# Performance work log

Measured on AMD Instinct MI355X. Metric: run time of the kernel, lower is better.

The kernel has to match this reference:

```python
import jax, jax.numpy as jnp
import numpy as np

VOCAB = 64
H = 64
B, L = 256, 2048


def setup_inputs() -> dict:
    key = jax.random.key(0)
    ks = jax.random.split(key, 12)
    s = 0.02
    return {
        "seq":   jax.random.randint(ks[0], (B, L), 0, VOCAB),
        "embed": jax.random.normal(ks[1], (VOCAB, H), jnp.float32) * s,
        "W1":    jax.random.normal(ks[2], (H, 2 * H), jnp.float32) * s,
        "b1":    jnp.zeros((2 * H,), jnp.float32),
        "W2":    jax.random.normal(ks[3], (2 * H, H), jnp.float32) * s,
        "b2":    jnp.zeros((H,), jnp.float32),
        "gamma": jnp.ones((H,), jnp.float32),
        "beta":  jnp.zeros((H,), jnp.float32),
        "Wr":    jax.random.normal(ks[4], (H, H), jnp.float32) * s,
        "br":    jnp.zeros((H,), jnp.float32),
        "Wo":    jax.random.normal(ks[5], (H, VOCAB), jnp.float32) * s,
        "bo":    jnp.zeros((VOCAB,), jnp.float32),
    }


def _layernorm(x, gamma, beta, eps=1e-5):
    mu = x.mean(-1, keepdims=True)
    var = ((x - mu) ** 2).mean(-1, keepdims=True)
    return (x - mu) * jax.lax.rsqrt(var + eps) * gamma + beta


def _encode(seq, embed, W1, b1, W2, b2, gamma, beta):
    h = embed[seq]                                   # [B, L, H]
    ff = jax.nn.relu(h @ W1 + b1) @ W2 + b2
    return _layernorm(h + ff, gamma, beta)


def _run_memory(hidden):
    # sequential energy-gated delta-rule update of fast-weight M [B,H,H]
    Bd, Ld, Hd = hidden.shape
    M0 = jnp.zeros((Bd, Hd, Hd), hidden.dtype)

    def step(carry, k):
        M, writes = carry
        v = k                                        # k == v == hidden[:, t]
        v_pred = jnp.einsum('bij,bj->bi', M, k)
        denom = (k * k).sum(-1, keepdims=True) + 1e-6
        delta_v = v - v_pred / denom
        dM = delta_v[:, :, None] * k[:, None, :]     # outer product [B,H,H]
        E_before = -0.5 * (M * M).sum((-2, -1))
        Mn = M + dM
        E_after = -0.5 * (Mn * Mn).sum((-2, -1))
        gate = E_after < E_before                    # [B] bool
        M = jnp.where(gate[:, None, None], Mn, M)
        writes = writes + gate.sum().astype(jnp.float32)
        return (M, writes), None

    keys = jnp.swapaxes(hidden[:, :-1, :], 0, 1)     # [L-1, B, H]
    (M, writes), _ = jax.lax.scan(step, (M0, jnp.float32(0.0)), keys)
    return M, writes


def reference(seq, embed, W1, b1, W2, b2, gamma, beta, Wr, br, Wo, bo):
    hidden = _encode(seq, embed, W1, b1, W2, b2, gamma, beta)
    Bd, Ld, Hd = hidden.shape
    M, writes = _run_memory(hidden)
    write_rate = writes / jnp.float32(Bd * (Ld - 1))
    query = hidden[:, -1, :]
    ctx = jnp.einsum('bij,bj->bi', M, query)
    logits = (ctx @ Wr + br) @ Wo + bo               # [B, VOCAB]
    return logits, write_rate
```

## Files before the change

kernel.cpp:

```cpp
#include <hip/hip_runtime.h>
#include <math.h>

#define VOCAB 64
#define H 64
#define BB 256
#define LL 2048

typedef float v2f __attribute__((ext_vector_type(2)));

#define PIN(x)  asm volatile("" : "+v"(x))
#define PIN4(f) asm volatile("" : "+v"(f.x), "+v"(f.y), "+v"(f.z), "+v"(f.w))

__device__ __forceinline__ float wave_sum_dpp(float x) {
  int t;
  float r = x;
  t = __builtin_amdgcn_update_dpp(0, __float_as_int(r), 0x111, 0xf, 0xf, true); r += __int_as_float(t);
  t = __builtin_amdgcn_update_dpp(0, __float_as_int(r), 0x112, 0xf, 0xf, true); r += __int_as_float(t);
  t = __builtin_amdgcn_update_dpp(0, __float_as_int(r), 0x114, 0xf, 0xf, true); r += __int_as_float(t);
  t = __builtin_amdgcn_update_dpp(0, __float_as_int(r), 0x118, 0xf, 0xf, true); r += __int_as_float(t);
  t = __builtin_amdgcn_update_dpp(0, __float_as_int(r), 0x142, 0xf, 0xf, true); r += __int_as_float(t);
  t = __builtin_amdgcn_update_dpp(0, __float_as_int(r), 0x143, 0xf, 0xf, true); r += __int_as_float(t);
  return __int_as_float(__builtin_amdgcn_readlane(__float_as_int(r), 63));
}

__global__ __launch_bounds__(64, 1) void encode_kernel(
    const float* __restrict__ embed, const float* __restrict__ W1,
    const float* __restrict__ b1, const float* __restrict__ W2,
    const float* __restrict__ b2, const float* __restrict__ gamma,
    const float* __restrict__ beta, float* __restrict__ table,
    float* __restrict__ kkg) {
  const int c = blockIdx.x;
  const int j = threadIdx.x;
  __shared__ float hs[H];
  __shared__ float zs[2 * H];
  const float h = embed[c * H + j];
  hs[j] = h;
  __syncthreads();
  float z0 = b1[j], z1 = b1[j + H];
#pragma unroll 8
  for (int i = 0; i < H; ++i) {
    const float hi = hs[i];
    z0 = fmaf(hi, W1[i * 2 * H + j], z0);
    z1 = fmaf(hi, W1[i * 2 * H + j + H], z1);
  }
  z0 = fmaxf(z0, 0.f);
  z1 = fmaxf(z1, 0.f);
  zs[j] = z0;
  zs[j + H] = z1;
  __syncthreads();
  float ff = b2[j];
#pragma unroll 8
  for (int m = 0; m < 2 * H; ++m) ff = fmaf(zs[m], W2[m * H + j], ff);
  const float x = h + ff;
  const float mu = wave_sum_dpp(x) * (1.f / 64.f);
  const float d = x - mu;
  const float var = wave_sum_dpp(d * d) * (1.f / 64.f);
  const float y = d * (1.f / sqrtf(var + 1e-5f)) * gamma[j] + beta[j];
  table[c * H + j] = y;
  const float s2 = wave_sum_dpp(y * y);
  if (j == 0) kkg[c] = s2;
}

#define STEP(T_IDX, RU, RD, RP)                                              \
  {                                                                          \
    const int cp = cnn;           \
    const int tpre = ((T_IDX) + 3 < LL) ? (T_IDX) + 3 : LL - 1;              \
    int cin = toks[tpre];                                                    \
    float scp = T[cp * H + lane];                                            \
    float kkp = KK[cp];                                                      \
    const float4* rp = (const float4*)(T + cp * H);                          \
    _Pragma("unroll")                                                        \
    for (int q = 0; q < 16; ++q) RP[q] = rp[q];                              \
    const float vp = (vpA.x + vpA.y) + (vpB.x + vpB.y);                      \
    const float dv = sc - vp / (kk + 1e-6f);                                 \
    const float aa = dv * (2.f * vp + dv * kk);                              \
    const float s = wave_sum_dpp(aa);                                        \
    const float dvg = s > 0.f ? dv : 0.f;                                    \
    wcount += s > 0.f ? 1.f : 0.f;                                           \
    const v2f dv2 = (v2f){dvg, dvg};                                         \
    v2f nA = (v2f){0.f, 0.f}, nB = (v2f){0.f, 0.f};                          \
    _Pragma("unroll")                                                        \
    for (int q = 0; q < 16; ++q) {                                           \
      const float4 kv4 = RU[q];                                              \
      const float4 kn4 = RD[q];                                              \
      const v2f kva = (v2f){kv4.x, kv4.y}, kvb = (v2f){kv4.z, kv4.w};        \
      const v2f kna = (v2f){kn4.x, kn4.y}, knb = (v2f){kn4.z, kn4.w};        \
      M2[2 * q]     = __builtin_elementwise_fma(dv2, kva, M2[2 * q]);        \
      M2[2 * q + 1] = __builtin_elementwise_fma(dv2, kvb, M2[2 * q + 1]);    \
      nA = __builtin_elementwise_fma(M2[2 * q],     kna, nA);                \
      nB = __builtin_elementwise_fma(M2[2 * q + 1], knb, nB);                \
    }                                                                        \
    vpA = nA; vpB = nB;                                                      \
    _Pragma("unroll")                                                        \
    for (int q = 0; q < 16; ++q) PIN4(RP[q]);                                \
    PIN(scp); PIN(kkp); PIN(cin);                                            \
    cn = cnn; cnn = cin;                                                     \
    sc = scn; kk = kkn; scn = scp; kkn = kkp;                                \
  }

__global__ __launch_bounds__(64, 1) void scan_kernel(
    const int* __restrict__ seq, const float* __restrict__ table,
    const float* __restrict__ kkg, const float* __restrict__ Wr,
    const float* __restrict__ br, const float* __restrict__ Wo,
    const float* __restrict__ bo, float* __restrict__ out,
    float* __restrict__ counts) {
  const int b = blockIdx.x;
  const int lane = threadIdx.x;
  __shared__ float T[H * VOCAB];
  __shared__ float KK[VOCAB];
  __shared__ int toks[LL];
  __shared__ float xv[H];

  {
    const float4* src = (const float4*)table;
    float4* dst = (float4*)T;
#pragma unroll
    for (int q = 0; q < 16; ++q) dst[q * 64 + lane] = src[q * 64 + lane];
    KK[lane] = kkg[lane];
    const int4* ssrc = (const int4*)(seq + (long)b * LL);
    int4* sdst = (int4*)toks;
#pragma unroll
    for (int q = 0; q < 8; ++q) sdst[q * 64 + lane] = ssrc[q * 64 + lane];
  }
  __syncthreads();

  v2f M2[32];
#pragma unroll
  for (int r = 0; r < 32; ++r) M2[r] = (v2f){0.f, 0.f};
  float wcount = 0.f;

  float4 RA[16], RB[16], RC[16];
  const int c0 = toks[0];
  int cn = toks[1], cnn = toks[2];
  float sc = T[c0 * H + lane], kk = KK[c0];
  float scn = T[cn * H + lane], kkn = KK[cn];
  {
    const float4* r0 = (const float4*)(T + c0 * H);
    const float4* r1 = (const float4*)(T + cn * H);
#pragma unroll
    for (int q = 0; q < 16; ++q) { RA[q] = r0[q]; RB[q] = r1[q]; }
#pragma unroll
    for (int q = 0; q < 16; ++q) { PIN4(RA[q]); PIN4(RB[q]); }
  }
  v2f vpA = (v2f){0.f, 0.f}, vpB = (v2f){0.f, 0.f};

  int t = 0;
  for (int it = 0; it < 682; ++it) {
    STEP(t, RA, RB, RC); ++t;
    STEP(t, RB, RC, RA); ++t;
    STEP(t, RC, RA, RB); ++t;
  }
  STEP(t, RA, RB, RC);

  xv[lane] = (vpA.x + vpA.y) + (vpB.x + vpB.y);
  __syncthreads();
  float t1 = br[lane];
#pragma unroll 8
  for (int i = 0; i < H; ++i) t1 = fmaf(xv[i], Wr[i * H + lane], t1);
  __syncthreads();
  xv[lane] = t1;
  __syncthreads();
  float lg = bo[lane];
#pragma unroll 8
  for (int m = 0; m < H; ++m) lg = fmaf(xv[m], Wo[m * H + lane], lg);
  out[(long)b * H + lane] = lg;
  if (lane == 0) counts[b] = wcount;
}

__global__ __launch_bounds__(256, 1) void finalize_kernel(const float* __restrict__ counts,
                                                          float* __restrict__ out) {
  const int lane = threadIdx.x;
  __shared__ float sbuf[BB];
  sbuf[lane] = counts[lane];
  __syncthreads();
  for (int off = BB / 2; off > 0; off >>= 1) {
    if (lane < off) sbuf[lane] += sbuf[lane + off];
    __syncthreads();
  }
  if (lane == 0) out[BB * H] = sbuf[0] / (float)(BB * (LL - 1));
}

extern "C" void kernel_launch(void* const* d_in, const int* in_sizes, int n_in,
                              void* d_out, int out_size, void* d_ws, size_t ws_size,
                              hipStream_t stream) {
  const int* seq      = (const int*)d_in[0];
  const float* embed  = (const float*)d_in[1];
  const float* W1     = (const float*)d_in[2];
  const float* b1     = (const float*)d_in[3];
  const float* W2     = (const float*)d_in[4];
  const float* b2     = (const float*)d_in[5];
  const float* gamma  = (const float*)d_in[6];
  const float* beta   = (const float*)d_in[7];
  const float* Wr     = (const float*)d_in[8];
  const float* br     = (const float*)d_in[9];
  const float* Wo     = (const float*)d_in[10];
  const float* bo     = (const float*)d_in[11];
  float* out = (float*)d_out;

  float* table  = (float*)d_ws;
  float* kkg    = table + VOCAB * H;
  float* counts = kkg + VOCAB;

  encode_kernel<<<VOCAB, H, 0, stream>>>(embed, W1, b1, W2, b2, gamma, beta, table, kkg);
  scan_kernel<<<BB, H, 0, stream>>>(seq, table, kkg, Wr, br, Wo, bo, out, counts);
  finalize_kernel<<<1, BB, 0, stream>>>(counts, out);
}
```

Baseline: 665.5 us.

## Pre-gather per-step key rows into global buffer and stream them in scan

Adds a gather kernel that materializes each batch's token-indexed hidden rows and squared norms into a large workspace buffer (B*L*H floats, about 128 MB). The scan kernel then streams the next row straight from global memory instead of doing dependent token lookups and LDS row reads, removing the token-to-row indirection from the serial loop. The cost is a large extra memory write and read, plus global-load latency on the critical path with only one step of prefetch. The old LDS path is kept as a fallback when the workspace is too small.

```diff
diff --git a/kernel.cpp b/kernel.cpp
--- a/kernel.cpp
+++ b/kernel.cpp
@@ -1,5 +1,6 @@
 #include <hip/hip_runtime.h>
 #include <math.h>
+#include <stdint.h>
 
 #define VOCAB 64
 #define H 64
@@ -61,9 +62,113 @@
   if (j == 0) kkg[c] = s2;
 }
 
-#define STEP(T_IDX, RU, RD, RP)                                              \
+__global__ __launch_bounds__(256, 1) void gather_kernel(
+    const int* __restrict__ seq, const float* __restrict__ table,
+    const float* __restrict__ kkg, float* __restrict__ rows,
+    float* __restrict__ kks) {
+  const int b = blockIdx.x;
+  const int tid = threadIdx.x;
+  __shared__ int tk[LL];
+  {
+    const int4* ssrc = (const int4*)(seq + (long)b * LL);
+    int4* sdst = (int4*)tk;
+#pragma unroll
+    for (int q = 0; q < 2; ++q) sdst[q * 256 + tid] = ssrc[q * 256 + tid];
+  }
+  __syncthreads();
+  const int j = tid & 63;
+  const int tq = tid >> 6;
+  float* dstb = rows + (long)b * LL * H;
+  float* kb = kks + (long)b * LL;
+  for (int t = tq; t < LL; t += 4) {
+    const int c = tk[t];
+    dstb[(long)t * H + j] = table[c * H + j];
+    if (j == 0) kb[t] = kkg[c];
+  }
+}
+
+#define STEP(T_IDX, R, X)                                                    \
   {                                                                          \
-    const int cp = cnn;           \
+    const long t2 = ((T_IDX) + 2 < LL) ? (T_IDX) + 2 : LL - 1;               \
+    const float4* xp = (const float4*)(rb + (long)((T_IDX) + 1) * H);        \
+    _Pragma("unroll")                                                        \
+    for (int q = 0; q < 16; ++q) X[q] = xp[q];                               \
+    const float scp = rb[t2 * H + lane];                                     \
+    const float kkp = kb[t2];                                                \
+    const float vp = (vpA.x + vpA.y) + (vpB.x + vpB.y);                      \
+    const float dv = sc - vp / (kk + 1e-6f);                                 \
+    const float aa = dv * (2.f * vp + dv * kk);                              \
+    const float s = wave_sum_dpp(aa);                                        \
+    const float dvg = s > 0.f ? dv : 0.f;                                    \
+    wcount += s > 0.f ? 1.f : 0.f;                                           \
+    const v2f dv2 = (v2f){dvg, dvg};                                         \
+    v2f nA = (v2f){0.f, 0.f}, nB = (v2f){0.f, 0.f};                          \
+    _Pragma("unroll")                                                        \
+    for (int q = 0; q < 16; ++q) {                                           \
+      const float4 kv4 = R[q];                                               \
+      const float4 kn4 = X[q];                                               \
+      const v2f kva = (v2f){kv4.x, kv4.y}, kvb = (v2f){kv4.z, kv4.w};        \
+      const v2f kna = (v2f){kn4.x, kn4.y}, knb = (v2f){kn4.z, kn4.w};        \
+      M2[2 * q]     = __builtin_elementwise_fma(dv2, kva, M2[2 * q]);        \
+      M2[2 * q + 1] = __builtin_elementwise_fma(dv2, kvb, M2[2 * q + 1]);    \
+      nA = __builtin_elementwise_fma(M2[2 * q],     kna, nA);                \
+      nB = __builtin_elementwise_fma(M2[2 * q + 1], knb, nB);                \
+    }                                                                        \
+    vpA = nA; vpB = nB;                                                      \
+    sc = scn; kk = kkn; scn = scp; kkn = kkp;                                \
+  }
+
+__global__ __launch_bounds__(64, 1) void scan_kernel_stream(
+    const float* __restrict__ rows, const float* __restrict__ kks,
+    const float* __restrict__ Wr, const float* __restrict__ br,
+    const float* __restrict__ Wo, const float* __restrict__ bo,
+    float* __restrict__ out, float* __restrict__ counts) {
+  const int b = blockIdx.x;
+  const int lane = threadIdx.x;
+  const float* rb = rows + (long)b * LL * H;
+  const float* kb = kks + (long)b * LL;
+  __shared__ float xv[H];
+
+  v2f M2[32];
+#pragma unroll
+  for (int r = 0; r < 32; ++r) M2[r] = (v2f){0.f, 0.f};
+  float wcount = 0.f;
+
+  float4 RA[16], RB[16];
+  {
+    const float4* r0 = (const float4*)rb;
+#pragma unroll
+    for (int q = 0; q < 16; ++q) RA[q] = r0[q];
+  }
+  float sc = rb[lane], kk = kb[0];
+  float scn = rb[H + lane], kkn = kb[1];
+  v2f vpA = (v2f){0.f, 0.f}, vpB = (v2f){0.f, 0.f};
+
+  int t = 0;
+  for (int it = 0; it < 1023; ++it) {
+    STEP(t, RA, RB); ++t;
+    STEP(t, RB, RA); ++t;
+  }
+  STEP(t, RA, RB);
+
+  xv[lane] = (vpA.x + vpA.y) + (vpB.x + vpB.y);
+  __syncthreads();
+  float t1 = br[lane];
+#pragma unroll 8
+  for (int i = 0; i < H; ++i) t1 = fmaf(xv[i], Wr[i * H + lane], t1);
+  __syncthreads();
+  xv[lane] = t1;
+  __syncthreads();
+  float lg = bo[lane];
+#pragma unroll 8
+  for (int m = 0; m < H; ++m) lg = fmaf(xv[m], Wo[m * H + lane], lg);
+  out[(long)b * H + lane] = lg;
+  if (lane == 0) counts[b] = wcount;
+}
+
+#define STEPL(T_IDX, RU, RD, RP)                                             \
+  {                                                                          \
+    const int cp = cnn;                                                      \
     const int tpre = ((T_IDX) + 3 < LL) ? (T_IDX) + 3 : LL - 1;              \
     int cin = toks[tpre];                                                    \
     float scp = T[cp * H + lane];                                            \
@@ -98,7 +203,7 @@
     sc = scn; kk = kkn; scn = scp; kkn = kkp;                                \
   }
 
-__global__ __launch_bounds__(64, 1) void scan_kernel(
+__global__ __launch_bounds__(64, 1) void scan_kernel_lds(
     const int* __restrict__ seq, const float* __restrict__ table,
     const float* __restrict__ kkg, const float* __restrict__ Wr,
     const float* __restrict__ br, const float* __restrict__ Wo,
@@ -110,7 +215,6 @@
   __shared__ float KK[VOCAB];
   __shared__ int toks[LL];
   __shared__ float xv[H];
-
   {
     const float4* src = (const float4*)table;
     float4* dst = (float4*)T;
@@ -123,12 +227,10 @@
     for (int q = 0; q < 8; ++q) sdst[q * 64 + lane] = ssrc[q * 64 + lane];
   }
   __syncthreads();
-
   v2f M2[32];
 #pragma unroll
   for (int r = 0; r < 32; ++r) M2[r] = (v2f){0.f, 0.f};
   float wcount = 0.f;
-
   float4 RA[16], RB[16], RC[16];
   const int c0 = toks[0];
   int cn = toks[1], cnn = toks[2];
@@ -143,15 +245,13 @@
     for (int q = 0; q < 16; ++q) { PIN4(RA[q]); PIN4(RB[q]); }
   }
   v2f vpA = (v2f){0.f, 0.f}, vpB = (v2f){0.f, 0.f};
-
   int t = 0;
   for (int it = 0; it < 682; ++it) {
-    STEP(t, RA, RB, RC); ++t;
-    STEP(t, RB, RC, RA); ++t;
-    STEP(t, RC, RA, RB); ++t;
-  }
-  STEP(t, RA, RB, RC);
-
+    STEPL(t, RA, RB, RC); ++t;
+    STEPL(t, RB, RC, RA); ++t;
+    STEPL(t, RC, RA, RB); ++t;
+  }
+  STEPL(t, RA, RB, RC);
   xv[lane] = (vpA.x + vpA.y) + (vpB.x + vpB.y);
   __syncthreads();
   float t1 = br[lane];
@@ -197,11 +297,20 @@
   const float* bo     = (const float*)d_in[11];
   float* out = (float*)d_out;
 
-  float* table  = (float*)d_ws;
+  float* ws = (float*)d_ws;
+  float* table  = ws;
   float* kkg    = table + VOCAB * H;
   float* counts = kkg + VOCAB;
+  float* rows   = ws + 8192;
+  float* kks    = rows + (size_t)BB * LL * H;
+  const size_t need = (8192 + (size_t)BB * LL * H + (size_t)BB * LL) * sizeof(float);
 
   encode_kernel<<<VOCAB, H, 0, stream>>>(embed, W1, b1, W2, b2, gamma, beta, table, kkg);
-  scan_kernel<<<BB, H, 0, stream>>>(seq, table, kkg, Wr, br, Wo, bo, out, counts);
+  if (ws_size >= need) {
+    gather_kernel<<<BB, 256, 0, stream>>>(seq, table, kkg, rows, kks);
+    scan_kernel_stream<<<BB, H, 0, stream>>>(rows, kks, Wr, br, Wo, bo, out, counts);
+  } else {
+    scan_kernel_lds<<<BB, H, 0, stream>>>(seq, table, kkg, Wr, br, Wo, bo, out, counts);
+  }
   finalize_kernel<<<1, BB, 0, stream>>>(counts, out);
 }
```

New measurement: 1.515 ms. +127.6%, slower.
